# Optimization experiments

Hardware: AMD Instinct MI355X
Metric: run time of the kernel (lower is better)

## Reference

```python
import jax, jax.numpy as jnp
import numpy as np

B, S, D, H = 2, 2048, 1024, 16
HD = D // H  # 64
NUM_BUCKETS = 32
MAX_DISTANCE = 128


def _relative_position_bucket(relative_position, num_buckets=NUM_BUCKETS, max_distance=MAX_DISTANCE):
    # bidirectional=True branch of the torch code
    num_buckets //= 2
    rel_buckets = (relative_position > 0).astype(jnp.int32) * num_buckets
    rp = jnp.abs(relative_position)
    max_exact = num_buckets // 2
    is_small = rp < max_exact
    # log-spaced buckets for larger distances
    rp_large = max_exact + (
        jnp.log(rp.astype(jnp.float32) / max_exact)
        / np.log(max_distance / max_exact)
        * (num_buckets - max_exact)
    ).astype(jnp.int32)
    rp_large = jnp.minimum(rp_large, num_buckets - 1)
    return rel_buckets + jnp.where(is_small, rp, rp_large)


def compute_bias(rel_bias, query_length, key_length):
    ctx = jnp.arange(query_length)[:, None]
    mem = jnp.arange(key_length)[None, :]
    buckets = _relative_position_bucket(mem - ctx)  # [q, k]
    values = rel_bias[buckets]                      # [q, k, h]
    return jnp.transpose(values, (2, 0, 1))[None]   # [1, h, q, k]


def setup_inputs() -> dict:
    key = jax.random.key(0)
    ks = jax.random.split(key, 6)
    scale = 1.0 / np.sqrt(D)
    return {
        "hidden_states": jax.random.normal(ks[0], (B, S, D), jnp.float32),
        "mask": jnp.ones((B, 1, 1, S), jnp.int32),
        "Wq": jax.random.normal(ks[1], (D, D), jnp.float32) * scale,
        "Wk": jax.random.normal(ks[2], (D, D), jnp.float32) * scale,
        "Wv": jax.random.normal(ks[3], (D, D), jnp.float32) * scale,
        "Wo": jax.random.normal(ks[4], (D, D), jnp.float32) * scale,
        "rel_bias": jax.random.normal(ks[5], (NUM_BUCKETS, H), jnp.float32),
    }


def reference(hidden_states, mask, Wq, Wk, Wv, Wo, rel_bias):
    b, s, _ = hidden_states.shape
    # projections (no bias), split heads -> [b, h, s, hd]
    def proj(x, W):
        return jnp.einsum("bsd,ed->bse", x, W).reshape(b, s, H, HD).transpose(0, 2, 1, 3)
    q = proj(hidden_states, Wq)
    k = proj(hidden_states, Wk)
    v = proj(hidden_states, Wv)
    # unscaled attention scores (T5 style): [b, h, s, s]
    scores = jnp.einsum("bhqd,bhkd->bhqk", q, k)
    position_bias = compute_bias(rel_bias, s, s)
    scores = scores + position_bias
    scores = jnp.where(mask == 0, jnp.float32(-1e9), scores)
    attn_weights = jax.nn.softmax(scores, axis=-1)
    # dropout p=0.0 (eval): identity
    attn_output = jnp.einsum("bhqk,bhkd->bhqd", attn_weights, v)
    attn_output = attn_output.transpose(0, 2, 1, 3).reshape(b, s, H * HD)
    attn_output = jnp.einsum("bse,de->bsd", attn_output, Wo)
    return attn_output, attn_weights, position_bias
```

## Files before the change

### kernel.cpp

```cpp
#include <hip/hip_runtime.h>

typedef __attribute__((ext_vector_type(8))) _Float16 half8;
typedef __attribute__((ext_vector_type(4))) _Float16 half4;
typedef __attribute__((ext_vector_type(4))) float f32x4;

#define SEQ 2048
#define DMODEL 1024
#define NHEAD 16
#define HEADD 64
#define NBH 32
#define LUTW 4096

__device__ __forceinline__ void nt_store_f4(float* p, f32x4 v) {
    __builtin_nontemporal_store(v, (f32x4*)p);
}

#define LDS_BAR() do {                                   \
    __builtin_amdgcn_sched_barrier(0);                   \
    asm volatile("s_waitcnt lgkmcnt(0)" ::: "memory");   \
    __builtin_amdgcn_sched_barrier(0);                   \
    __builtin_amdgcn_s_barrier();                        \
    __builtin_amdgcn_sched_barrier(0);                   \
} while (0)

__device__ __forceinline__ int rel_bucket(int rel) {
    int ret = (rel > 0) ? 16 : 0;
    int rp = rel < 0 ? -rel : rel;
    if (rp < 8) return ret + rp;
    float x = logf((float)rp * 0.125f) / 2.7725887f * 8.0f;
    int v = 8 + (int)x;
    v = v < 15 ? v : 15;
    return ret + v;
}

__global__ __launch_bounds__(256) void prep_kernel(const float* __restrict__ hs,
                                                   const float* __restrict__ Wq,
                                                   const float* __restrict__ Wk,
                                                   const float* __restrict__ Wv,
                                                   const float* __restrict__ Wo,
                                                   const float* __restrict__ rel_bias,
                                                   _Float16* __restrict__ Xh,
                                                   _Float16* __restrict__ Wqh,
                                                   _Float16* __restrict__ Wkh,
                                                   _Float16* __restrict__ Wvh,
                                                   _Float16* __restrict__ Woh,
                                                   float* __restrict__ lut) {
    int bid = blockIdx.x;
    if (bid < 4096) {
        const float* in;
        _Float16* out;
        int base;
        if (bid < 2048)      { in = hs; out = Xh;  base = bid; }
        else if (bid < 2560) { in = Wq; out = Wqh; base = bid - 2048; }
        else if (bid < 3072) { in = Wk; out = Wkh; base = bid - 2560; }
        else if (bid < 3584) { in = Wv; out = Wvh; base = bid - 3072; }
        else                 { in = Wo; out = Woh; base = bid - 3584; }
        int i = (base * 256 + threadIdx.x) * 8;
        f32x4 a = *(const f32x4*)(in + i);
        f32x4 b = *(const f32x4*)(in + i + 4);
        half8 r;
        r[0] = (_Float16)a[0]; r[1] = (_Float16)a[1];
        r[2] = (_Float16)a[2]; r[3] = (_Float16)a[3];
        r[4] = (_Float16)b[0]; r[5] = (_Float16)b[1];
        r[6] = (_Float16)b[2]; r[7] = (_Float16)b[3];
        *(half8*)(out + i) = r;
    } else {
        int i = (bid - 4096) * 256 + threadIdx.x;
        int h = i >> 12;
        int idx = i & (LUTW - 1);
        int rel = idx - 2047;
        int b = rel_bucket(rel);
        lut[i] = rel_bias[b * NHEAD + h];
    }
}

__global__ __launch_bounds__(256) void proj3_kernel(const _Float16* __restrict__ Xh,
                                                    const _Float16* __restrict__ Wqh,
                                                    const _Float16* __restrict__ Wkh,
                                                    const _Float16* __restrict__ Wvh,
                                                    _Float16* __restrict__ Qh,
                                                    _Float16* __restrict__ Kh,
                                                    _Float16* __restrict__ Vt,
                                                    const float* __restrict__ lut,
                                                    float* __restrict__ posb) {
    int z = blockIdx.z;
    if (z == 3) {
        int flat = blockIdx.y * 8 + blockIdx.x;
        const size_t total = (size_t)NHEAD * SEQ * SEQ / 4;
        for (size_t idx = (size_t)flat * 256 + threadIdx.x; idx < total; idx += 65536) {
            size_t e = idx * 4;
            int k = (int)(e & 2047);
            int q = (int)((e >> 11) & 2047);
            int h = (int)(e >> 22);
            f32x4 v;
            __builtin_memcpy(&v, lut + h * LUTW + (k - q + 2047), 16);
            nt_store_f4(posb + e, v);
        }
        return;
    }
    const _Float16* B = (z == 0) ? Wqh : (z == 1) ? Wkh : Wvh;
    int l = threadIdx.x & 63, w = threadIdx.x >> 6;
    int row0 = blockIdx.y * 128 + (w >> 1) * 64;
    int col0 = blockIdx.x * 128 + (w & 1) * 64;
    int ar = l & 15, ak = (l >> 4) * 8;
    f32x4 acc[4][4] = {};
    for (int k0 = 0; k0 < DMODEL; k0 += 32) {
        half8 af[4], bf[4];
#pragma unroll
        for (int mi = 0; mi < 4; mi++)
            af[mi] = *(const half8*)(Xh + (size_t)(row0 + mi * 16 + ar) * DMODEL + k0 + ak);
#pragma unroll
        for (int ni = 0; ni < 4; ni++)
            bf[ni] = *(const half8*)(B + (size_t)(col0 + ni * 16 + ar) * DMODEL + k0 + ak);
#pragma unroll
        for (int mi = 0; mi < 4; mi++)
#pragma unroll
            for (int ni = 0; ni < 4; ni++)
                acc[mi][ni] = __builtin_amdgcn_mfma_f32_16x16x32_f16(af[mi], bf[ni], acc[mi][ni], 0, 0, 0);
    }
    int cr = (l >> 4) * 4, cc = l & 15;
    if (z < 2) {
        _Float16* C = z == 0 ? Qh : Kh;
#pragma unroll
        for (int mi = 0; mi < 4; mi++)
#pragma unroll
            for (int ni = 0; ni < 4; ni++) {
                int c = col0 + ni * 16 + cc;
#pragma unroll
                for (int j = 0; j < 4; j++)
                    C[(size_t)(row0 + mi * 16 + cr + j) * DMODEL + c] = (_Float16)acc[mi][ni][j];
            }
    } else {
#pragma unroll
        for (int mi = 0; mi < 4; mi++)
#pragma unroll
            for (int ni = 0; ni < 4; ni++) {
                int c = col0 + ni * 16 + cc;
                int h = c >> 6, hd = c & 63;
                int r = row0 + mi * 16 + cr;
                int b = r >> 11, s0 = r & 2047;
                half4 pk;
#pragma unroll
                for (int j = 0; j < 4; j++) pk[j] = (_Float16)acc[mi][ni][j];
                *(half4*)(Vt + (size_t)((b * NHEAD + h) * HEADD + hd) * SEQ + s0) = pk;
            }
    }
}

__global__ __launch_bounds__(256) void outgemm_kernel(const _Float16* __restrict__ A,
                                                      const _Float16* __restrict__ B,
                                                      float* __restrict__ C) {
    int l = threadIdx.x & 63, w = threadIdx.x >> 6;
    int row0 = blockIdx.y * 128 + (w >> 1) * 64;
    int col0 = blockIdx.x * 128 + (w & 1) * 64;
    int ar = l & 15, ak = (l >> 4) * 8;
    f32x4 acc[4][4] = {};
    for (int k0 = 0; k0 < DMODEL; k0 += 32) {
        half8 af[4], bf[4];
#pragma unroll
        for (int mi = 0; mi < 4; mi++)
            af[mi] = *(const half8*)(A + (size_t)(row0 + mi * 16 + ar) * DMODEL + k0 + ak);
#pragma unroll
        for (int ni = 0; ni < 4; ni++)
            bf[ni] = *(const half8*)(B + (size_t)(col0 + ni * 16 + ar) * DMODEL + k0 + ak);
#pragma unroll
        for (int mi = 0; mi < 4; mi++)
#pragma unroll
            for (int ni = 0; ni < 4; ni++)
                acc[mi][ni] = __builtin_amdgcn_mfma_f32_16x16x32_f16(af[mi], bf[ni], acc[mi][ni], 0, 0, 0);
    }
    int cr = (l >> 4) * 4, cc = l & 15;
#pragma unroll
    for (int mi = 0; mi < 4; mi++)
#pragma unroll
        for (int ni = 0; ni < 4; ni++) {
            int c = col0 + ni * 16 + cc;
#pragma unroll
            for (int j = 0; j < 4; j++)
                C[(size_t)(row0 + mi * 16 + cr + j) * DMODEL + c] = acc[mi][ni][j];
        }
}

__global__ __launch_bounds__(512) void attn_kernel(const _Float16* __restrict__ Q,
                                                   const _Float16* __restrict__ Kg,
                                                   const _Float16* __restrict__ Vg,
                                                   const float* __restrict__ lut,
                                                   const int* __restrict__ mask,
                                                   float* __restrict__ wts,
                                                   _Float16* __restrict__ attn0) {
    __shared__ _Float16 Kt[64][68];
    __shared__ _Float16 Vl[64][68];
    __shared__ _Float16 Pl[8][16][72];
    int tid = threadIdx.x;
    int l = tid & 63, wid = tid >> 6;
    int wsub = wid & 3, psel = wid >> 2;
    int bid = blockIdx.x;
    int xcd = bid & 7, idx = bid >> 3;
    int bh = (idx >> 3) * 8 + xcd;
    int qp = (idx & 7) * 2 + psel;
    int b = bh >> 4, h = bh & 15;
    int qbaseA = qp * 64 + wsub * 16;
    int qbaseB = qbaseA + 1024;
    size_t hoff = (size_t)(b * SEQ) * DMODEL + h * HEADD;
    int ar = l & 15, g = l >> 4, ak = g * 8;
    const float* luth = lut + h * LUTW;
    float* ob = wts + (size_t)bh * SEQ * SEQ;
    int qA = qbaseA + ar;
    int qB = qbaseB + ar;

    int sr = tid >> 3, sc = (tid & 7) * 8;
    const _Float16* Ksrc = Kg + hoff + sc;
    const _Float16* Vsrc = Vg + ((size_t)bh * HEADD + sr) * SEQ + sc;

    half8 qfA[2], qfB[2];
#pragma unroll
    for (int kk = 0; kk < 2; kk++) {
        qfA[kk] = *(const half8*)(Q + hoff + (size_t)qA * DMODEL + kk * 32 + ak);
        qfB[kk] = *(const half8*)(Q + hoff + (size_t)qB * DMODEL + kk * 32 + ak);
    }

    half8 s0 = *(const half8*)(Ksrc + (size_t)sr * DMODEL);
    float mA = -3e38f, lsumA = 0.f;
    float mB = -3e38f, lsumB = 0.f;
    for (int k0 = 0; k0 < SEQ; k0 += 64) {
        *(half8*)&Kt[sr][sc] = s0;
        LDS_BAR();
        int4 mk[4];
        f32x4 lbA[4], lbB[4];
#pragma unroll
        for (int ni = 0; ni < 4; ni++) {
            int kcol = k0 + ni * 16 + g * 4;
            mk[ni] = *(const int4*)(mask + b * SEQ + kcol);
            __builtin_memcpy(&lbA[ni], luth + kcol - qA + 2047, 16);
            __builtin_memcpy(&lbB[ni], luth + kcol - qB + 2047, 16);
        }
        if (k0 + 64 < SEQ)
            s0 = *(const half8*)(Ksrc + (size_t)(k0 + 64 + sr) * DMODEL);
        f32x4 accA[4] = {}, accB[4] = {};
#pragma unroll
        for (int ni = 0; ni < 4; ni++)
#pragma unroll
            for (int kk = 0; kk < 2; kk++) {
                half8 kf = *(const half8*)&Kt[ni * 16 + ar][kk * 32 + ak];
                accA[ni] = __builtin_amdgcn_mfma_f32_16x16x32_f16(kf, qfA[kk], accA[ni], 0, 0, 0);
                accB[ni] = __builtin_amdgcn_mfma_f32_16x16x32_f16(kf, qfB[kk], accB[ni], 0, 0, 0);
            }
        LDS_BAR();
        {
            float vv[16];
#pragma unroll
            for (int ni = 0; ni < 4; ni++) {
                const int* mp = (const int*)&mk[ni];
#pragma unroll
                for (int j = 0; j < 4; j++)
                    vv[ni * 4 + j] = mp[j] ? (accA[ni][j] + lbA[ni][j]) : -1e9f;
            }
            float t8[8];
#pragma unroll
            for (int t = 0; t < 8; t++) t8[t] = fmaxf(vv[t], vv[t + 8]);
            float t4a = fmaxf(t8[0], t8[4]), t4b = fmaxf(t8[1], t8[5]);
            float t4c = fmaxf(t8[2], t8[6]), t4d = fmaxf(t8[3], t8[7]);
            float vmax = fmaxf(fmaxf(t4a, t4b), fmaxf(t4c, t4d));
            float mn = fmaxf(mA, vmax);
            float scale = __expf(mA - mn);
            float e[16];
#pragma unroll
            for (int t = 0; t < 16; t++) e[t] = __expf(vv[t] - mn);
            float s8[8];
#pragma unroll
            for (int t = 0; t < 8; t++) s8[t] = e[t] + e[t + 8];
            float s4a = s8[0] + s8[4], s4b = s8[1] + s8[5];
            float s4c = s8[2] + s8[6], s4d = s8[3] + s8[7];
            lsumA = lsumA * scale + (s4a + s4b) + (s4c + s4d);
            mA = mn;
        }
        {
            float vv[16];
#pragma unroll
            for (int ni = 0; ni < 4; ni++) {
                const int* mp = (const int*)&mk[ni];
#pragma unroll
                for (int j = 0; j < 4; j++)
                    vv[ni * 4 + j] = mp[j] ? (accB[ni][j] + lbB[ni][j]) : -1e9f;
            }
            float t8[8];
#pragma unroll
            for (int t = 0; t < 8; t++) t8[t] = fmaxf(vv[t], vv[t + 8]);
            float t4a = fmaxf(t8[0], t8[4]), t4b = fmaxf(t8[1], t8[5]);
            float t4c = fmaxf(t8[2], t8[6]), t4d = fmaxf(t8[3], t8[7]);
            float vmax = fmaxf(fmaxf(t4a, t4b), fmaxf(t4c, t4d));
            float mn = fmaxf(mB, vmax);
            float scale = __expf(mB - mn);
            float e[16];
#pragma unroll
            for (int t = 0; t < 16; t++) e[t] = __expf(vv[t] - mn);
            float s8[8];
#pragma unroll
            for (int t = 0; t < 8; t++) s8[t] = e[t] + e[t + 8];
            float s4a = s8[0] + s8[4], s4b = s8[1] + s8[5];
            float s4c = s8[2] + s8[6], s4d = s8[3] + s8[7];
            lsumB = lsumB * scale + (s4a + s4b) + (s4c + s4d);
            mB = mn;
        }
    }
    half8 t0 = *(const half8*)(Ksrc + (size_t)sr * DMODEL);
    half8 v0 = *(const half8*)(Vsrc);
#pragma unroll
    for (int off2 = 16; off2 <= 32; off2 <<= 1) {
        float mo = __shfl_xor(mA, off2);
        float lo = __shfl_xor(lsumA, off2);
        float mn = fmaxf(mA, mo);
        lsumA = lsumA * __expf(mA - mn) + lo * __expf(mo - mn);
        mA = mn;
        mo = __shfl_xor(mB, off2);
        lo = __shfl_xor(lsumB, off2);
        mn = fmaxf(mB, mo);
        lsumB = lsumB * __expf(mB - mn) + lo * __expf(mo - mn);
        mB = mn;
    }
    float invlA = 1.0f / lsumA;
    float invlB = 1.0f / lsumB;
    LDS_BAR();

    f32x4 oaccA[4] = {}, oaccB[4] = {};
    for (int k0 = 0; k0 < SEQ; k0 += 64) {
        *(half8*)&Kt[sr][sc] = t0;
        *(half8*)&Vl[sr][sc] = v0;
        LDS_BAR();
        int4 mk[4];
        f32x4 lbA[4], lbB[4];
#pragma unroll
        for (int ni = 0; ni < 4; ni++) {
            int kcol = k0 + ni * 16 + g * 4;
            mk[ni] = *(const int4*)(mask + b * SEQ + kcol);
            __builtin_memcpy(&lbA[ni], luth + kcol - qA + 2047, 16);
            __builtin_memcpy(&lbB[ni], luth + kcol - qB + 2047, 16);
        }
        if (k0 + 64 < SEQ) {
            t0 = *(const half8*)(Ksrc + (size_t)(k0 + 64 + sr) * DMODEL);
            v0 = *(const half8*)(Vsrc + k0 + 64);
        }
        f32x4 accA[4] = {}, accB[4] = {};
#pragma unroll
        for (int ni = 0; ni < 4; ni++)
#pragma unroll
            for (int kk = 0; kk < 2; kk++) {
                half8 kf = *(const half8*)&Kt[ni * 16 + ar][kk * 32 + ak];
                accA[ni] = __builtin_amdgcn_mfma_f32_16x16x32_f16(kf, qfA[kk], accA[ni], 0, 0, 0);
                accB[ni] = __builtin_amdgcn_mfma_f32_16x16x32_f16(kf, qfB[kk], accB[ni], 0, 0, 0);
            }
#pragma unroll
        for (int ni = 0; ni < 4; ni++) {
            int kcol = k0 + ni * 16 + g * 4;
            const int* mp = (const int*)&mk[ni];
            f32x4 wv;
#pragma unroll
            for (int j = 0; j < 4; j++) {
                float v = mp[j] ? (accA[ni][j] + lbA[ni][j]) : -1e9f;
                wv[j] = __expf(v - mA) * invlA;
            }
            nt_store_f4(ob + (size_t)qA * SEQ + kcol, wv);
            half4 ph;
#pragma unroll
            for (int j = 0; j < 4; j++) ph[j] = (_Float16)wv[j];
            *(half4*)&Pl[wid][ar][ni * 16 + g * 4] = ph;
        }
#pragma unroll
        for (int kk2 = 0; kk2 < 2; kk2++) {
            half8 pa = *(half8*)&Pl[wid][ar][kk2 * 32 + g * 8];
#pragma unroll
            for (int ni = 0; ni < 4; ni++) {
                half8 vf = *(const half8*)&Vl[ni * 16 + ar][kk2 * 32 + g * 8];
                oaccA[ni] = __builtin_amdgcn_mfma_f32_16x16x32_f16(pa, vf, oaccA[ni], 0, 0, 0);
            }
        }
#pragma unroll
        for (int ni = 0; ni < 4; ni++) {
            int kcol = k0 + ni * 16 + g * 4;
            const int* mp = (const int*)&mk[ni];
            f32x4 wv;
#pragma unroll
            for (int j = 0; j < 4; j++) {
                float v = mp[j] ? (accB[ni][j] + lbB[ni][j]) : -1e9f;
                wv[j] = __expf(v - mB) * invlB;
            }
            nt_store_f4(ob + (size_t)qB * SEQ + kcol, wv);
            half4 ph;
#pragma unroll
            for (int j = 0; j < 4; j++) ph[j] = (_Float16)wv[j];
            *(half4*)&Pl[wid][ar][ni * 16 + g * 4] = ph;
        }
#pragma unroll
        for (int kk2 = 0; kk2 < 2; kk2++) {
            half8 pa = *(half8*)&Pl[wid][ar][kk2 * 32 + g * 8];
#pragma unroll
            for (int ni = 0; ni < 4; ni++) {
                half8 vf = *(const half8*)&Vl[ni * 16 + ar][kk2 * 32 + g * 8];
                oaccB[ni] = __builtin_amdgcn_mfma_f32_16x16x32_f16(pa, vf, oaccB[ni], 0, 0, 0);
            }
        }
        LDS_BAR();
    }
#pragma unroll
    for (int ni = 0; ni < 4; ni++)
#pragma unroll
        for (int j = 0; j < 4; j++) {
            attn0[(size_t)(b * SEQ + qbaseA + g * 4 + j) * DMODEL + h * HEADD + ni * 16 + ar] =
                (_Float16)oaccA[ni][j];
            attn0[(size_t)(b * SEQ + qbaseB + g * 4 + j) * DMODEL + h * HEADD + ni * 16 + ar] =
                (_Float16)oaccB[ni][j];
        }
}

extern "C" void kernel_launch(void* const* d_in, const int* in_sizes, int n_in,
                              void* d_out, int out_size, void* d_ws, size_t ws_size,
                              hipStream_t stream) {
    const float* hs = (const float*)d_in[0];
    const int* mask = (const int*)d_in[1];
    const float* Wq = (const float*)d_in[2];
    const float* Wk = (const float*)d_in[3];
    const float* Wv = (const float*)d_in[4];
    const float* Wo = (const float*)d_in[5];
    const float* rel_bias = (const float*)d_in[6];

    float* out_attn = (float*)d_out;
    float* out_wts = out_attn + (size_t)2 * SEQ * DMODEL;
    float* out_posb = out_wts + (size_t)NBH * SEQ * SEQ;

    char* ws = (char*)d_ws;
    size_t off = 0;
    auto carve = [&](size_t bytes) { void* p = ws + off; off += (bytes + 255) & ~(size_t)255; return p; };
    _Float16* Xh  = (_Float16*)carve((size_t)2 * SEQ * DMODEL * 2);
    _Float16* Wqh = (_Float16*)carve((size_t)DMODEL * DMODEL * 2);
    _Float16* Wkh = (_Float16*)carve((size_t)DMODEL * DMODEL * 2);
    _Float16* Wvh = (_Float16*)carve((size_t)DMODEL * DMODEL * 2);
    _Float16* Woh = (_Float16*)carve((size_t)DMODEL * DMODEL * 2);
    _Float16* Qh  = (_Float16*)carve((size_t)2 * SEQ * DMODEL * 2);
    _Float16* Kh  = (_Float16*)carve((size_t)2 * SEQ * DMODEL * 2);
    _Float16* Vt  = (_Float16*)carve((size_t)NBH * HEADD * SEQ * 2);
    _Float16* A0h = (_Float16*)carve((size_t)2 * SEQ * DMODEL * 2);
    float* lut    = (float*)carve((size_t)NHEAD * LUTW * 4);

    prep_kernel<<<4352, 256, 0, stream>>>(hs, Wq, Wk, Wv, Wo, rel_bias,
                                          Xh, Wqh, Wkh, Wvh, Woh, lut);

    dim3 pg(DMODEL / 128, (2 * SEQ) / 128, 4);
    proj3_kernel<<<pg, 256, 0, stream>>>(Xh, Wqh, Wkh, Wvh, Qh, Kh, Vt, lut, out_posb);

    attn_kernel<<<256, 512, 0, stream>>>(Qh, Kh, Vt, lut, mask, out_wts, A0h);

    dim3 og(DMODEL / 128, (2 * SEQ) / 128);
    outgemm_kernel<<<og, 256, 0, stream>>>(A0h, Woh, out_attn);
}
```

Measured before the change: 432.3 us.

## Stage GEMM tiles in LDS via direct global-to-LDS loads for projections

The QKV projection and output GEMMs now load 128x32 A and B tiles cooperatively into shared memory using global_load_lds, and each wave reads its MFMA fragments from LDS. Before, every wave loaded its own fragments straight from global memory, so operands shared between waves were fetched more than once. The exchange is two block barriers per k-step with a single buffer and no prefetch, which may expose load latency.

Result: faster. 385.5 us, median of 2 (-10.8%).

```diff
diff --git a/kernel.cpp b/kernel.cpp
--- a/kernel.cpp
+++ b/kernel.cpp
@@ -14,6 +14,10 @@
 __device__ __forceinline__ void nt_store_f4(float* p, f32x4 v) {
     __builtin_nontemporal_store(v, (f32x4*)p);
 }
+
+#define GLOAD16(gp, lp) __builtin_amdgcn_global_load_lds(                    \
+    (const __attribute__((address_space(1))) void*)(gp),                     \
+    (__attribute__((address_space(3))) void*)(lp), 16, 0, 0)
 
 #define LDS_BAR() do {                                   \
     __builtin_amdgcn_sched_barrier(0);                   \
@@ -74,6 +78,47 @@
     }
 }
 
+__device__ __forceinline__ void gemm_body_gll(const _Float16* __restrict__ A,
+                                              const _Float16* __restrict__ B,
+                                              _Float16* As, _Float16* Bs,
+                                              int row0, int col0,
+                                              f32x4 (&acc)[4][4]) {
+    int tid = threadIdx.x;
+    int l = tid & 63, wid = tid >> 6;
+    int ar = l & 15, ak = (l >> 4) * 8;
+    int mrow = (wid >> 1) * 64, ncol = (wid & 1) * 64;
+    int srow = wid * 32 + (l >> 2);
+    int scol = (l & 3) * 8;
+    const _Float16* ga0 = A + (size_t)(row0 + srow) * DMODEL + scol;
+    const _Float16* ga1 = A + (size_t)(row0 + srow + 16) * DMODEL + scol;
+    const _Float16* gb0 = B + (size_t)(col0 + srow) * DMODEL + scol;
+    const _Float16* gb1 = B + (size_t)(col0 + srow + 16) * DMODEL + scol;
+    _Float16* la0 = As + wid * 1024 + l * 8;
+    _Float16* la1 = As + wid * 1024 + 512 + l * 8;
+    _Float16* lb0 = Bs + wid * 1024 + l * 8;
+    _Float16* lb1 = Bs + wid * 1024 + 512 + l * 8;
+    for (int k0 = 0; k0 < DMODEL; k0 += 32) {
+        GLOAD16(ga0 + k0, la0);
+        GLOAD16(ga1 + k0, la1);
+        GLOAD16(gb0 + k0, lb0);
+        GLOAD16(gb1 + k0, lb1);
+        __syncthreads();
+        half8 af[4], bf[4];
+#pragma unroll
+        for (int mi = 0; mi < 4; mi++)
+            af[mi] = *(const half8*)(As + (mrow + mi * 16 + ar) * 32 + ak);
+#pragma unroll
+        for (int ni = 0; ni < 4; ni++)
+            bf[ni] = *(const half8*)(Bs + (ncol + ni * 16 + ar) * 32 + ak);
+#pragma unroll
+        for (int mi = 0; mi < 4; mi++)
+#pragma unroll
+            for (int ni = 0; ni < 4; ni++)
+                acc[mi][ni] = __builtin_amdgcn_mfma_f32_16x16x32_f16(af[mi], bf[ni], acc[mi][ni], 0, 0, 0);
+        __syncthreads();
+    }
+}
+
 __global__ __launch_bounds__(256) void proj3_kernel(const _Float16* __restrict__ Xh,
                                                     const _Float16* __restrict__ Wqh,
                                                     const _Float16* __restrict__ Wkh,
@@ -83,6 +128,8 @@
                                                     _Float16* __restrict__ Vt,
                                                     const float* __restrict__ lut,
                                                     float* __restrict__ posb) {
+    __shared__ _Float16 As[128 * 32];
+    __shared__ _Float16 Bs[128 * 32];
     int z = blockIdx.z;
     if (z == 3) {
         int flat = blockIdx.y * 8 + blockIdx.x;
@@ -99,25 +146,12 @@
         return;
     }
     const _Float16* B = (z == 0) ? Wqh : (z == 1) ? Wkh : Wvh;
-    int l = threadIdx.x & 63, w = threadIdx.x >> 6;
-    int row0 = blockIdx.y * 128 + (w >> 1) * 64;
-    int col0 = blockIdx.x * 128 + (w & 1) * 64;
-    int ar = l & 15, ak = (l >> 4) * 8;
+    int row0 = blockIdx.y * 128, col0 = blockIdx.x * 128;
     f32x4 acc[4][4] = {};
-    for (int k0 = 0; k0 < DMODEL; k0 += 32) {
-        half8 af[4], bf[4];
-#pragma unroll
-        for (int mi = 0; mi < 4; mi++)
-            af[mi] = *(const half8*)(Xh + (size_t)(row0 + mi * 16 + ar) * DMODEL + k0 + ak);
-#pragma unroll
-        for (int ni = 0; ni < 4; ni++)
-            bf[ni] = *(const half8*)(B + (size_t)(col0 + ni * 16 + ar) * DMODEL + k0 + ak);
-#pragma unroll
-        for (int mi = 0; mi < 4; mi++)
-#pragma unroll
-            for (int ni = 0; ni < 4; ni++)
-                acc[mi][ni] = __builtin_amdgcn_mfma_f32_16x16x32_f16(af[mi], bf[ni], acc[mi][ni], 0, 0, 0);
-    }
+    gemm_body_gll(Xh, B, As, Bs, row0, col0, acc);
+    int l = threadIdx.x & 63, wid = threadIdx.x >> 6;
+    int r0 = row0 + (wid >> 1) * 64;
+    int c0 = col0 + (wid & 1) * 64;
     int cr = (l >> 4) * 4, cc = l & 15;
     if (z < 2) {
         _Float16* C = z == 0 ? Qh : Kh;
@@ -125,19 +159,19 @@
         for (int mi = 0; mi < 4; mi++)
 #pragma unroll
             for (int ni = 0; ni < 4; ni++) {
-                int c = col0 + ni * 16 + cc;
+                int c = c0 + ni * 16 + cc;
 #pragma unroll
                 for (int j = 0; j < 4; j++)
-                    C[(size_t)(row0 + mi * 16 + cr + j) * DMODEL + c] = (_Float16)acc[mi][ni][j];
+                    C[(size_t)(r0 + mi * 16 + cr + j) * DMODEL + c] = (_Float16)acc[mi][ni][j];
             }
     } else {
 #pragma unroll
         for (int mi = 0; mi < 4; mi++)
 #pragma unroll
             for (int ni = 0; ni < 4; ni++) {
-                int c = col0 + ni * 16 + cc;
+                int c = c0 + ni * 16 + cc;
                 int h = c >> 6, hd = c & 63;
-                int r = row0 + mi * 16 + cr;
+                int r = r0 + mi * 16 + cr;
                 int b = r >> 11, s0 = r & 2047;
                 half4 pk;
 #pragma unroll
@@ -150,34 +184,23 @@
 __global__ __launch_bounds__(256) void outgemm_kernel(const _Float16* __restrict__ A,
                                                       const _Float16* __restrict__ B,
                                                       float* __restrict__ C) {
-    int l = threadIdx.x & 63, w = threadIdx.x >> 6;
-    int row0 = blockIdx.y * 128 + (w >> 1) * 64;
-    int col0 = blockIdx.x * 128 + (w & 1) * 64;
-    int ar = l & 15, ak = (l >> 4) * 8;
+    __shared__ _Float16 As[128 * 32];
+    __shared__ _Float16 Bs[128 * 32];
+    int row0 = blockIdx.y * 128, col0 = blockIdx.x * 128;
     f32x4 acc[4][4] = {};
-    for (int k0 = 0; k0 < DMODEL; k0 += 32) {
-        half8 af[4], bf[4];
-#pragma unroll
-        for (int mi = 0; mi < 4; mi++)
-            af[mi] = *(const half8*)(A + (size_t)(row0 + mi * 16 + ar) * DMODEL + k0 + ak);
-#pragma unroll
-        for (int ni = 0; ni < 4; ni++)
-            bf[ni] = *(const half8*)(B + (size_t)(col0 + ni * 16 + ar) * DMODEL + k0 + ak);
-#pragma unroll
-        for (int mi = 0; mi < 4; mi++)
-#pragma unroll
-            for (int ni = 0; ni < 4; ni++)
-                acc[mi][ni] = __builtin_amdgcn_mfma_f32_16x16x32_f16(af[mi], bf[ni], acc[mi][ni], 0, 0, 0);
-    }
+    gemm_body_gll(A, B, As, Bs, row0, col0, acc);
+    int l = threadIdx.x & 63, wid = threadIdx.x >> 6;
+    int r0 = row0 + (wid >> 1) * 64;
+    int c0 = col0 + (wid & 1) * 64;
     int cr = (l >> 4) * 4, cc = l & 15;
 #pragma unroll
     for (int mi = 0; mi < 4; mi++)
 #pragma unroll
         for (int ni = 0; ni < 4; ni++) {
-            int c = col0 + ni * 16 + cc;
+            int c = c0 + ni * 16 + cc;
 #pragma unroll
             for (int j = 0; j < 4; j++)
-                C[(size_t)(row0 + mi * 16 + cr + j) * DMODEL + c] = acc[mi][ni][j];
+                C[(size_t)(r0 + mi * 16 + cr + j) * DMODEL + c] = acc[mi][ni][j];
         }
 }
 
```
